# Kernel optimization log

Hardware: AMD Instinct MI355X
Metric: run time of the kernel (lower is better)

## Reference

```python
import jax, jax.numpy as jnp
import numpy as np

SEQ, B, IN_DIM = 100, 2048, 64
MID_I, LATENT, V_MID, V_LAT, MID_O, OUT_DIM = 60, 20, 800, 50, 800, 512


def _lstm_cell(x, h, c, wih, whh, bih, bhh):
    # PyTorch gate order: i, f, g, o
    g = x @ wih.T + h @ whh.T + bih + bhh
    i, f, gg, o = jnp.split(g, 4, axis=-1)
    c = jax.nn.sigmoid(f) * c + jax.nn.sigmoid(i) * jnp.tanh(gg)
    h = jax.nn.sigmoid(o) * jnp.tanh(c)
    return h, c


def _lstm_seq(xs, wih, whh, bih, bhh, hid):
    b = xs.shape[1]
    init = (jnp.zeros((b, hid), xs.dtype), jnp.zeros((b, hid), xs.dtype))
    def step(carry, xt):
        h, c = _lstm_cell(xt, carry[0], carry[1], wih, whh, bih, bhh)
        return (h, c), h
    _, outs = jax.lax.scan(step, init, xs)
    return outs  # (seq, B, hid)


def setup_inputs() -> dict:
    key = jax.random.key(0)
    ks = iter(jax.random.split(key, 40))
    w = lambda shape: jax.random.normal(next(ks), shape, jnp.float32) * 0.05
    p = {}
    p['x'] = jax.random.normal(next(ks), (SEQ, B, IN_DIM), jnp.float32)
    p['fc1_wih'] = w((4 * MID_I, IN_DIM)); p['fc1_whh'] = w((4 * MID_I, MID_I))
    p['fc1_bih'] = w((4 * MID_I,)); p['fc1_bhh'] = w((4 * MID_I,))
    p['fc21_wih'] = w((4 * LATENT, MID_I)); p['fc21_whh'] = w((4 * LATENT, LATENT))
    p['fc21_bih'] = w((4 * LATENT,)); p['fc21_bhh'] = w((4 * LATENT,))
    p['lin1_w'] = w((V_MID, LATENT * SEQ)); p['lin1_b'] = w((V_MID,))
    p['lin2_w'] = w((V_LAT, V_MID)); p['lin2_b'] = w((V_LAT,))
    p['idlin_w'] = w((V_LAT, V_LAT)); p['idlin_b'] = w((V_LAT,))
    p['down1_w'] = w((LATENT, V_LAT)); p['down1_b'] = w((LATENT,))
    p['down2_w'] = w((LATENT, OUT_DIM)); p['down2_b'] = w((LATENT,))
    p['l3_wih'] = w((4 * V_LAT, LATENT)); p['l3_whh'] = w((4 * V_LAT, V_LAT))
    p['l3_bih'] = w((4 * V_LAT,)); p['l3_bhh'] = w((4 * V_LAT,))
    p['l4_wih'] = w((4 * MID_O, V_LAT)); p['l4_whh'] = w((4 * MID_O, MID_O))
    p['l4_bih'] = w((4 * MID_O,)); p['l4_bhh'] = w((4 * MID_O,))
    p['l5_wih'] = w((4 * OUT_DIM, MID_O)); p['l5_whh'] = w((4 * OUT_DIM, OUT_DIM))
    p['l5_bih'] = w((4 * OUT_DIM,)); p['l5_bhh'] = w((4 * OUT_DIM,))
    return p


def reference(x, fc1_wih, fc1_whh, fc1_bih, fc1_bhh,
              fc21_wih, fc21_whh, fc21_bih, fc21_bhh,
              lin1_w, lin1_b, lin2_w, lin2_b,
              idlin_w, idlin_b, down1_w, down1_b, down2_w, down2_b,
              l3_wih, l3_whh, l3_bih, l3_bhh,
              l4_wih, l4_whh, l4_bih, l4_bhh,
              l5_wih, l5_whh, l5_bih, l5_bhh):
    seq, b, _ = x.shape
    # encode
    h1 = jax.nn.relu(_lstm_seq(x, fc1_wih, fc1_whh, fc1_bih, fc1_bhh, MID_I))
    out21 = _lstm_seq(h1, fc21_wih, fc21_whh, fc21_bih, fc21_bhh, LATENT)
    flat = jnp.transpose(out21, (1, 2, 0)).reshape(b, -1)  # (B, latent*seq)
    mu = jax.nn.relu(flat @ lin1_w.T + lin1_b)
    mu = jax.nn.relu(mu @ lin2_w.T + lin2_b)  # (B, v_latent)
    # decode
    h_t = mu
    c_t = mu @ idlin_w.T + idlin_b
    out = mu @ down1_w.T + down1_b
    h2 = jnp.zeros((b, MID_O), mu.dtype); c2 = jnp.zeros((b, MID_O), mu.dtype)
    h3 = jnp.zeros((b, OUT_DIM), mu.dtype); c3 = jnp.zeros((b, OUT_DIM), mu.dtype)
    def step(carry, _):
        h_t, c_t, h2, c2, h3, c3, out = carry
        h_t, c_t = _lstm_cell(out, h_t, c_t, l3_wih, l3_whh, l3_bih, l3_bhh)
        h2, c2 = _lstm_cell(h_t, h2, c2, l4_wih, l4_whh, l4_bih, l4_bhh)
        h3, c3 = _lstm_cell(h2, h3, c3, l5_wih, l5_whh, l5_bih, l5_bhh)
        out = h3 @ down2_w.T + down2_b
        return (h_t, c_t, h2, c2, h3, c3, out), h3
    _, muTheta = jax.lax.scan(step, (h_t, c_t, h2, c2, h3, c3, out), None, length=seq)
    return muTheta, mu
```

## Files before the change

### kernel.cpp

```cpp
#include <hip/hip_runtime.h>
#include <cstdint>
#include <cstddef>

#define SEQ     100
#define BATCH   2048
#define IN_DIM  64
#define MID_I   60
#define LATENT  20
#define V_MID   800
#define V_LAT   50
#define MID_O   800
#define OUT_DIM 512

#define KP4  896
#define KP5  1344
#define KPL1 2048

using f32x4  = __attribute__((ext_vector_type(4))) float;
using u16x8  = __attribute__((ext_vector_type(8))) unsigned short;
using bf16x8 = __attribute__((ext_vector_type(8))) __bf16;
typedef _Float16 f16;
typedef _Float16 f16x8 __attribute__((ext_vector_type(8)));

__device__ __forceinline__ unsigned short f2bf(float x){
    unsigned u = __builtin_bit_cast(unsigned, x);
    u += 0x7FFFu + ((u >> 16) & 1u);
    return (unsigned short)(u >> 16);
}
__device__ __forceinline__ float bf2f(unsigned short b){
    unsigned u = ((unsigned)b) << 16; return __builtin_bit_cast(float, u);
}
__device__ __forceinline__ float sigm(float x){ return 1.f/(1.f+__expf(-x)); }
__device__ __forceinline__ float tanh_f(float x){ return 1.f - 2.f/(__expf(2.f*x)+1.f); }

typedef const __attribute__((address_space(1))) unsigned int* gas_ptr;
typedef __attribute__((address_space(3))) unsigned int* las_ptr;
__device__ __forceinline__ void gld16(const void* g, char* l) {
    __builtin_amdgcn_global_load_lds((gas_ptr)g, (las_ptr)l, 16, 0, 0);
}

constexpr int BM = 64, BN = 64, BK = 16;
template<bool RELU_A1, bool RELU_OUT>
__global__ __launch_bounds__(256)
void gemm2k(const float* __restrict__ A1, int K1,
            const float* __restrict__ A2, int K2,
            const float* __restrict__ W1, const float* __restrict__ W2,
            const float* __restrict__ b1, const float* __restrict__ b2,
            float* __restrict__ C, int M, int N)
{
    __shared__ float As[BK][BM + 1];
    __shared__ float Bs[BK][BN + 1];
    const int tx = threadIdx.x & 15;
    const int ty = threadIdx.x >> 4;
    const int n0 = blockIdx.x * BN;
    const int m0 = blockIdx.y * BM;

    float acc[4][4] = {};

    for (int src = 0; src < 2; ++src) {
        const float* A = src ? A2 : A1;
        const float* W = src ? W2 : W1;
        const int    K = src ? K2 : K1;
        if (A == nullptr || K == 0) continue;
        for (int k0 = 0; k0 < K; k0 += BK) {
            #pragma unroll
            for (int i = 0; i < 4; ++i) {
                int idx = threadIdx.x + i * 256;
                int k = idx & 15, m = idx >> 4;
                int gm = m0 + m, gk = k0 + k;
                float v = 0.f;
                if (gm < M && gk < K) v = A[(size_t)gm * K + gk];
                if (RELU_A1 && src == 0) v = fmaxf(v, 0.f);
                As[k][m] = v;
            }
            #pragma unroll
            for (int i = 0; i < 4; ++i) {
                int idx = threadIdx.x + i * 256;
                int k = idx & 15, n = idx >> 4;
                int gn = n0 + n, gk = k0 + k;
                float v = 0.f;
                if (gn < N && gk < K) v = W[(size_t)gn * K + gk];
                Bs[k][n] = v;
            }
            __syncthreads();
            #pragma unroll
            for (int kk = 0; kk < BK; ++kk) {
                float a[4], b[4];
                #pragma unroll
                for (int i = 0; i < 4; ++i) a[i] = As[kk][ty + i * 16];
                #pragma unroll
                for (int j = 0; j < 4; ++j) b[j] = Bs[kk][tx + j * 16];
                #pragma unroll
                for (int i = 0; i < 4; ++i)
                    #pragma unroll
                    for (int j = 0; j < 4; ++j)
                        acc[i][j] += a[i] * b[j];
            }
            __syncthreads();
        }
    }

    #pragma unroll
    for (int i = 0; i < 4; ++i) {
        int gm = m0 + ty + i * 16;
        if (gm >= M) continue;
        #pragma unroll
        for (int j = 0; j < 4; ++j) {
            int gn = n0 + tx + j * 16;
            if (gn >= N) continue;
            float v = acc[i][j];
            if (b1) v += b1[gn];
            if (b2) v += b2[gn];
            if (RELU_OUT) v = fmaxf(v, 0.f);
            C[(size_t)gm * N + gn] = v;
        }
    }
}

template<bool RELU>
__global__ __launch_bounds__(256, 2)
void gemm_mfma0(const unsigned short* __restrict__ Ah, const unsigned short* __restrict__ Al,
                const unsigned short* __restrict__ Bh, const unsigned short* __restrict__ Bl,
                int Kp, int Nstore, const float* __restrict__ bi, float* __restrict__ Cout)
{
    __shared__ __align__(16) char smem[32768];
    const int tid  = threadIdx.x;
    const int lane = tid & 63;
    const int wid  = tid >> 6;
    const int m0   = blockIdx.y * 128;
    const int n0   = blockIdx.x * 128;
    const int wr   = (wid >> 1) << 6;
    const int wc   = (wid & 1) << 6;
    const int fr   = lane & 15;
    const int fg   = lane >> 4;
    const int slotR = ((fg ^ (fr & 3)) << 4);

    const int r0 = 32 * wid + (lane >> 2);
    const int sl = (((lane & 3) ^ ((lane >> 2) & 3)) << 3);
    const unsigned short* gA0h = Ah + (size_t)(m0 + r0)      * Kp + sl;
    const unsigned short* gA1h = Ah + (size_t)(m0 + r0 + 16) * Kp + sl;
    const unsigned short* gA0l = Al + (size_t)(m0 + r0)      * Kp + sl;
    const unsigned short* gA1l = Al + (size_t)(m0 + r0 + 16) * Kp + sl;
    const unsigned short* gB0h = Bh + (size_t)(n0 + r0)      * Kp + sl;
    const unsigned short* gB1h = Bh + (size_t)(n0 + r0 + 16) * Kp + sl;
    const unsigned short* gB0l = Bl + (size_t)(n0 + r0)      * Kp + sl;
    const unsigned short* gB1l = Bl + (size_t)(n0 + r0 + 16) * Kp + sl;
    char* lA0h = smem +     0 + (2 * wid    ) * 1024;
    char* lA1h = smem +     0 + (2 * wid + 1) * 1024;
    char* lA0l = smem +  8192 + (2 * wid    ) * 1024;
    char* lA1l = smem +  8192 + (2 * wid + 1) * 1024;
    char* lB0h = smem + 16384 + (2 * wid    ) * 1024;
    char* lB1h = smem + 16384 + (2 * wid + 1) * 1024;
    char* lB0l = smem + 24576 + (2 * wid    ) * 1024;
    char* lB1l = smem + 24576 + (2 * wid + 1) * 1024;

    f32x4 acc[4][4];
    #pragma unroll
    for (int i = 0; i < 4; ++i)
        #pragma unroll
        for (int j = 0; j < 4; ++j) acc[i][j] = (f32x4){0.f, 0.f, 0.f, 0.f};

    for (int k0 = 0; k0 < Kp; k0 += 32) {
        __syncthreads();
        gld16(gA0h + k0, lA0h); gld16(gA1h + k0, lA1h);
        gld16(gA0l + k0, lA0l); gld16(gA1l + k0, lA1l);
        gld16(gB0h + k0, lB0h); gld16(gB1h + k0, lB1h);
        gld16(gB0l + k0, lB0l); gld16(gB1l + k0, lB1l);
        __syncthreads();

        bf16x8 ah[4], al[4];
        #pragma unroll
        for (int i = 0; i < 4; ++i) {
            int ro = (wr + i * 16 + fr) * 64 + slotR;
            ah[i] = *(const bf16x8*)(smem +        ro);
            al[i] = *(const bf16x8*)(smem + 8192 + ro);
        }
        #pragma unroll
        for (int j = 0; j < 4; ++j) {
            int ro = (wc + j * 16 + fr) * 64 + slotR;
            bf16x8 fbh = *(const bf16x8*)(smem + 16384 + ro);
            bf16x8 fbl = *(const bf16x8*)(smem + 24576 + ro);
            #pragma unroll
            for (int i = 0; i < 4; ++i) {
                acc[i][j] = __builtin_amdgcn_mfma_f32_16x16x32_bf16(ah[i], fbh, acc[i][j], 0, 0, 0);
                acc[i][j] = __builtin_amdgcn_mfma_f32_16x16x32_bf16(ah[i], fbl, acc[i][j], 0, 0, 0);
                acc[i][j] = __builtin_amdgcn_mfma_f32_16x16x32_bf16(al[i], fbh, acc[i][j], 0, 0, 0);
            }
        }
    }

    #pragma unroll
    for (int j = 0; j < 4; ++j) {
        int gc = n0 + wc + j * 16 + fr;
        if (gc >= Nstore) continue;
        float badd = bi[gc];
        #pragma unroll
        for (int i = 0; i < 4; ++i)
            #pragma unroll
            for (int r = 0; r < 4; ++r) {
                int gr = m0 + wr + i * 16 + fg * 4 + r;
                float v = acc[i][j][r] + badd;
                if (RELU) v = fmaxf(v, 0.f);
                Cout[(size_t)gr * Nstore + gc] = v;
            }
    }
}

template<int MODE>
__global__ __launch_bounds__(256, 3)
void gemm_dec(const f16* __restrict__ A, const f16* __restrict__ W,
              int Kp, int NK, int H, int NBYX,
              const float* __restrict__ bp,
              float* __restrict__ cstate,
              f16* __restrict__ wr1, int st1, int off1,
              f16* __restrict__ wr2, int st2, int off2,
              float* __restrict__ out_t)
{
    __shared__ __align__(16) char smem[49152];
    const int xcd = blockIdx.x & 7;
    const int ii  = blockIdx.x >> 3;
    const int by  = xcd * NBYX + (ii % NBYX);
    const int bx  = ii / NBYX;
    const int m0 = by * 128;
    const int n0 = bx * 128;

    const int tid  = threadIdx.x;
    const int lane = tid & 63;
    const int wid  = tid >> 6;
    const int wm   = wid >> 1;
    const int wn   = wid & 1;
    const int fr   = lane & 15;
    const int fg   = lane >> 4;
    const int swz  = (fg ^ (fr & 3) ^ ((fr >> 2) & 1)) * 16;

    const int rbase = 32 * wid;
    const int lrow  = lane >> 2;
    const int chnk  = (lane & 3) ^ ((lane >> 2) & 3) ^ ((lane >> 4) & 1);
    const f16* sA0 = A + (size_t)(m0 + rbase + lrow)      * Kp + chnk * 8;
    const f16* sA1 = A + (size_t)(m0 + rbase + 16 + lrow) * Kp + chnk * 8;
    const f16* sW0 = W + (size_t)(n0 + rbase + lrow)      * Kp + chnk * 8;
    const f16* sW1 = W + (size_t)(n0 + rbase + 16 + lrow) * Kp + chnk * 8;

    f32x4 acc[4][4];
    #pragma unroll
    for (int i = 0; i < 4; ++i)
        #pragma unroll
        for (int j = 0; j < 4; ++j) acc[i][j] = (f32x4){0.f, 0.f, 0.f, 0.f};

    auto stage = [&](int t, int buf) {
        const int kb = t * 32;
        char* bb = smem + buf * 16384;
        gld16(sA0 + kb, bb + rbase * 64);
        gld16(sA1 + kb, bb + (rbase + 16) * 64);
        gld16(sW0 + kb, bb + 8192 + rbase * 64);
        gld16(sW1 + kb, bb + 8192 + (rbase + 16) * 64);
    };

    stage(0, 0);
    stage(1, 1);

    int buf = 0;
    for (int t = 0; t < NK; ++t) {
        if (t + 1 < NK) asm volatile("s_waitcnt vmcnt(4)" ::: "memory");
        else            asm volatile("s_waitcnt vmcnt(0)" ::: "memory");
        __builtin_amdgcn_s_barrier();
        if (t + 2 < NK) stage(t + 2, (buf + 2) % 3);
        const char* bb = smem + buf * 16384;
        f16x8 af[4];
        #pragma unroll
        for (int i = 0; i < 4; ++i)
            af[i] = *(const f16x8*)(bb + (64 * wm + 16 * i + fr) * 64 + swz);
        #pragma unroll
        for (int j = 0; j < 4; ++j) {
            f16x8 vw = *(const f16x8*)(bb + 8192 + (64 * wn + 16 * j + fr) * 64 + swz);
            #pragma unroll
            for (int i = 0; i < 4; ++i)
                acc[i][j] = __builtin_amdgcn_mfma_f32_16x16x32_f16(af[i], vw, acc[i][j], 0, 0, 0);
        }
        buf = (buf + 1) % 3;
    }

    float* gt = (float*)smem;
    const int u32 = tid & 31;
    const int r8  = tid >> 5;
    const int unit = (n0 >> 2) + u32;
    const f32x4 bv = ((const f32x4*)bp)[unit];

    #pragma unroll
    for (int half = 0; half < 2; ++half) {
        __syncthreads();
        if (wm == half) {
            #pragma unroll
            for (int i = 0; i < 4; ++i)
                #pragma unroll
                for (int j = 0; j < 4; ++j)
                    #pragma unroll
                    for (int r = 0; r < 4; ++r)
                        gt[(16*i + 4*fg + r) * 132 + 64*wn + 16*j + fr] = acc[i][j][r];
        }
        __syncthreads();
        #pragma unroll
        for (int kk = 0; kk < 8; ++kk) {
            const int lr  = 8 * kk + r8;
            const int row = m0 + 64 * half + lr;
            f32x4 g = *(const f32x4*)(gt + lr * 132 + u32 * 4);
            float gi = g[0] + bv[0], gf = g[1] + bv[1];
            float gg = g[2] + bv[2], go = g[3] + bv[3];
            size_t ci = (size_t)row * H + unit;
            float cn = sigm(gf) * cstate[ci] + sigm(gi) * tanh_f(gg);
            float hn = sigm(go) * tanh_f(cn);
            cstate[ci] = cn;
            f16 hh = (f16)hn;
            wr1[(size_t)row * st1 + off1 + unit] = hh;
            if (MODE == 1) wr2[(size_t)row * st2 + off2 + unit] = hh;
            if (MODE == 2) out_t[(size_t)row * H + unit] = hn;
        }
    }
}

__global__ void split_pack_lin1(const float* __restrict__ src,
                                unsigned short* __restrict__ dh, unsigned short* __restrict__ dl)
{
    int idx = blockIdx.x * blockDim.x + threadIdx.x;
    if (idx >= V_MID * LATENT * SEQ) return;
    int n = idx / (LATENT * SEQ), c = idx - n * (LATENT * SEQ);
    int l = c / SEQ, s = c - l * SEQ;
    float x = src[idx];
    unsigned short h = f2bf(x);
    size_t d = (size_t)n * KPL1 + s * LATENT + l;
    dh[d] = h;
    dl[d] = f2bf(x - bf2f(h));
}

__global__ void split_pack_rows(const float* __restrict__ src, int total, int K, int Kp,
                                unsigned short* __restrict__ dh, unsigned short* __restrict__ dl)
{
    int idx = blockIdx.x * blockDim.x + threadIdx.x;
    if (idx >= total) return;
    int n = idx / K, k = idx - n * K;
    float x = src[idx];
    unsigned short h = f2bf(x);
    size_t d = (size_t)n * Kp + k;
    dh[d] = h;
    dl[d] = f2bf(x - bf2f(h));
}

__global__ void pack_f16(const float* __restrict__ src, int total, int K, int Kp,
                         int coff, int HU, f16* __restrict__ dh)
{
    int idx = blockIdx.x * blockDim.x + threadIdx.x;
    if (idx >= total) return;
    int n = idx / K, k = idx - n * K;
    int p = (n % HU) * 4 + n / HU;
    dh[(size_t)p * Kp + coff + k] = (f16)src[idx];
}

__global__ void pack_flat_f16(const float* __restrict__ src, int total, f16* __restrict__ d)
{
    int idx = blockIdx.x * blockDim.x + threadIdx.x;
    if (idx < total) d[idx] = (f16)src[idx];
}

__global__ void bias_pack(const float* __restrict__ bih, const float* __restrict__ bhh,
                          int H, float* __restrict__ bp)
{
    int idx = blockIdx.x * blockDim.x + threadIdx.x;
    if (idx >= 4 * H) return;
    int g = idx / H, u = idx - g * H;
    bp[u * 4 + g] = bih[idx] + bhh[idx];
}

__global__ void bias_sum(const float* __restrict__ a, const float* __restrict__ b,
                         int n, float* __restrict__ d)
{
    int idx = blockIdx.x * blockDim.x + threadIdx.x;
    if (idx < n) d[idx] = a[idx] + b[idx];
}

__global__ __launch_bounds__(256)
void enc_rec1(const float* __restrict__ xp, int T,
              const float* __restrict__ whh,
              float* __restrict__ hbuf, float* __restrict__ cbuf,
              unsigned short* __restrict__ h1h, unsigned short* __restrict__ h1l)
{
    __shared__ float Wt[60][240];
    __shared__ float hs[4][60];
    for (int idx = threadIdx.x; idx < 240 * 60; idx += 256) {
        int n = idx / 60, k = idx % 60;
        Wt[k][n] = whh[idx];
    }
    int wid = threadIdx.x >> 6, lane = threadIdx.x & 63;
    int b = blockIdx.x * 4 + wid;
    float h = 0.f, c = 0.f;
    if (lane < 60) {
        h = hbuf[(size_t)b * 60 + lane];
        c = cbuf[(size_t)b * 60 + lane];
        hs[wid][lane] = h;
    }
    __syncthreads();
    for (int t = 0; t < T; ++t) {
        if (lane < 60) {
            const float* xr = xp + ((size_t)t * BATCH + b) * 240;
            float gi = xr[lane], gf = xr[60 + lane], gg = xr[120 + lane], go = xr[180 + lane];
            for (int k = 0; k < 60; ++k) {
                float v = hs[wid][k];
                gi += v * Wt[k][lane];
                gf += v * Wt[k][60 + lane];
                gg += v * Wt[k][120 + lane];
                go += v * Wt[k][180 + lane];
            }
            float cn = sigm(gf) * c + sigm(gi) * tanh_f(gg);
            float hn = sigm(go) * tanh_f(cn);
            c = cn; h = hn;
            float rh = fmaxf(hn, 0.f);
            unsigned short hh = f2bf(rh);
            size_t d = ((size_t)t * BATCH + b) * 64 + lane;
            h1h[d] = hh;
            h1l[d] = f2bf(rh - bf2f(hh));
        }
        __syncthreads();
        if (lane < 60) hs[wid][lane] = h;
        __syncthreads();
    }
    if (lane < 60) {
        hbuf[(size_t)b * 60 + lane] = h;
        cbuf[(size_t)b * 60 + lane] = c;
    }
}

__global__ __launch_bounds__(256)
void enc_rec21(const float* __restrict__ xp, int T, int t0,
               const float* __restrict__ whh,
               float* __restrict__ hbuf, float* __restrict__ cbuf,
               unsigned short* __restrict__ fh, unsigned short* __restrict__ fl)
{
    __shared__ float Wt[20][80];
    __shared__ float hs[4][20];
    for (int idx = threadIdx.x; idx < 80 * 20; idx += 256) {
        int n = idx / 20, k = idx % 20;
        Wt[k][n] = whh[idx];
    }
    int wid = threadIdx.x >> 6, lane = threadIdx.x & 63;
    int b = blockIdx.x * 4 + wid;
    float h = 0.f, c = 0.f;
    if (lane < 20) {
        h = hbuf[(size_t)b * 20 + lane];
        c = cbuf[(size_t)b * 20 + lane];
        hs[wid][lane] = h;
    }
    __syncthreads();
    for (int t = 0; t < T; ++t) {
        if (lane < 20) {
            const float* xr = xp + ((size_t)t * BATCH + b) * 80;
            float gi = xr[lane], gf = xr[20 + lane], gg = xr[40 + lane], go = xr[60 + lane];
            for (int k = 0; k < 20; ++k) {
                float v = hs[wid][k];
                gi += v * Wt[k][lane];
                gf += v * Wt[k][20 + lane];
                gg += v * Wt[k][40 + lane];
                go += v * Wt[k][60 + lane];
            }
            float cn = sigm(gf) * c + sigm(gi) * tanh_f(gg);
            float hn = sigm(go) * tanh_f(cn);
            c = cn; h = hn;
            int col = (t0 + t) * 20 + lane;
            unsigned short hh = f2bf(hn);
            fh[(size_t)b * KPL1 + col] = hh;
            fl[(size_t)b * KPL1 + col] = f2bf(hn - bf2f(hh));
        }
        __syncthreads();
        if (lane < 20) hs[wid][lane] = h;
        __syncthreads();
    }
    if (lane < 20) {
        hbuf[(size_t)b * 20 + lane] = h;
        cbuf[(size_t)b * 20 + lane] = c;
    }
}

__global__ __launch_bounds__(256)
void dec_l3(const float* __restrict__ outb,
            const float* __restrict__ wih,
            const float* __restrict__ whh,
            const float* __restrict__ bih, const float* __restrict__ bhh,
            float* __restrict__ h_t, float* __restrict__ c_t,
            f16* __restrict__ a4)
{
    __shared__ float Wt[70][200];
    __shared__ float xin[4][70];
    for (int idx = threadIdx.x; idx < 200 * 20; idx += 256) {
        int n = idx / 20, k = idx % 20;
        Wt[k][n] = wih[idx];
    }
    for (int idx = threadIdx.x; idx < 200 * 50; idx += 256) {
        int n = idx / 50, k = idx % 50;
        Wt[20 + k][n] = whh[idx];
    }
    int wid = threadIdx.x >> 6, lane = threadIdx.x & 63;
    int b = blockIdx.x * 4 + wid;
    if (lane < 20) xin[wid][lane]      = outb[(size_t)b * 20 + lane];
    if (lane < 50) xin[wid][20 + lane] = h_t[(size_t)b * 50 + lane];
    __syncthreads();
    if (lane < 50) {
        float gi = bih[lane] + bhh[lane];
        float gf = bih[50 + lane] + bhh[50 + lane];
        float gg = bih[100 + lane] + bhh[100 + lane];
        float go = bih[150 + lane] + bhh[150 + lane];
        for (int k = 0; k < 70; ++k) {
            float v = xin[wid][k];
            gi += v * Wt[k][lane];
            gf += v * Wt[k][50 + lane];
            gg += v * Wt[k][100 + lane];
            go += v * Wt[k][150 + lane];
        }
        float cold = c_t[(size_t)b * 50 + lane];
        float cn = sigm(gf) * cold + sigm(gi) * tanh_f(gg);
        float hn = sigm(go) * tanh_f(cn);
        c_t[(size_t)b * 50 + lane] = cn;
        h_t[(size_t)b * 50 + lane] = hn;
        a4[(size_t)b * KP4 + lane] = (f16)hn;
    }
}

__global__ __launch_bounds__(512)
void dec_step3(const float* __restrict__ h3prev,
               const f16* __restrict__ w2p, const float* __restrict__ b2,
               const float* __restrict__ wih, const float* __restrict__ whh,
               const float* __restrict__ bih, const float* __restrict__ bhh,
               float* __restrict__ h_t, float* __restrict__ c_t,
               f16* __restrict__ a4)
{
    __shared__ f16   w2s[20][512];
    __shared__ float W3[70][200];
    __shared__ float xb[8][80];
    const int tid  = threadIdx.x;
    const int lane = tid & 63;
    const int w    = tid >> 6;
    const int row  = blockIdx.x * 8 + w;

    for (int idx = tid; idx < 20 * 512; idx += 512)
        w2s[idx >> 9][idx & 511] = w2p[idx];
    for (int idx = tid; idx < 200 * 20; idx += 512) {
        int n = idx / 20, k = idx - n * 20;
        W3[k][n] = wih[idx];
    }
    for (int idx = tid; idx < 200 * 50; idx += 512) {
        int n = idx / 50, k = idx - n * 50;
        W3[20 + k][n] = whh[idx];
    }
    if (lane < 50) xb[w][20 + lane] = h_t[(size_t)row * 50 + lane];

    float hreg[8];
    const float* hrow = h3prev + (size_t)row * 512;
    #pragma unroll
    for (int c = 0; c < 8; ++c) hreg[c] = hrow[lane + 64 * c];
    __syncthreads();

    #pragma unroll 4
    for (int n = 0; n < 20; ++n) {
        float s = 0.f;
        #pragma unroll
        for (int c = 0; c < 8; ++c) s += hreg[c] * (float)w2s[n][lane + 64 * c];
        #pragma unroll
        for (int o = 32; o; o >>= 1) s += __shfl_xor(s, o);
        if (lane == 0) xb[w][n] = s + b2[n];
    }
    __syncthreads();

    if (lane < 50) {
        const int u = lane;
        float gi = bih[u] + bhh[u];
        float gf = bih[50 + u] + bhh[50 + u];
        float gg = bih[100 + u] + bhh[100 + u];
        float go = bih[150 + u] + bhh[150 + u];
        for (int k = 0; k < 70; ++k) {
            float v = xb[w][k];
            gi += v * W3[k][u];
            gf += v * W3[k][50 + u];
            gg += v * W3[k][100 + u];
            go += v * W3[k][150 + u];
        }
        size_t ci = (size_t)row * 50 + u;
        float cn = sigm(gf) * c_t[ci] + sigm(gi) * tanh_f(gg);
        float hn = sigm(go) * tanh_f(cn);
        c_t[ci] = cn;
        h_t[ci] = hn;
        a4[(size_t)row * KP4 + u] = (f16)hn;
    }
}

extern "C" void kernel_launch(void* const* d_in, const int* in_sizes, int n_in,
                              void* d_out_v, int out_size, void* d_ws, size_t ws_size,
                              hipStream_t stream)
{
    const float* x        = (const float*)d_in[0];
    const float* fc1_wih  = (const float*)d_in[1];
    const float* fc1_whh  = (const float*)d_in[2];
    const float* fc1_bih  = (const float*)d_in[3];
    const float* fc1_bhh  = (const float*)d_in[4];
    const float* fc21_wih = (const float*)d_in[5];
    const float* fc21_whh = (const float*)d_in[6];
    const float* fc21_bih = (const float*)d_in[7];
    const float* fc21_bhh = (const float*)d_in[8];
    const float* lin1_w   = (const float*)d_in[9];
    const float* lin1_b   = (const float*)d_in[10];
    const float* lin2_w   = (const float*)d_in[11];
    const float* lin2_b   = (const float*)d_in[12];
    const float* idlin_w  = (const float*)d_in[13];
    const float* idlin_b  = (const float*)d_in[14];
    const float* down1_w  = (const float*)d_in[15];
    const float* down1_b  = (const float*)d_in[16];
    const float* down2_w  = (const float*)d_in[17];
    const float* down2_b  = (const float*)d_in[18];
    const float* l3_wih   = (const float*)d_in[19];
    const float* l3_whh   = (const float*)d_in[20];
    const float* l3_bih   = (const float*)d_in[21];
    const float* l3_bhh   = (const float*)d_in[22];
    const float* l4_wih   = (const float*)d_in[23];
    const float* l4_whh   = (const float*)d_in[24];
    const float* l4_bih   = (const float*)d_in[25];
    const float* l4_bhh   = (const float*)d_in[26];
    const float* l5_wih   = (const float*)d_in[27];
    const float* l5_whh   = (const float*)d_in[28];
    const float* l5_bih   = (const float*)d_in[29];
    const float* l5_bhh   = (const float*)d_in[30];
    float* out = (float*)d_out_v;

    char* base = (char*)d_ws;
    size_t off = 0;
    auto alloc = [&](size_t bytes) -> void* {
        off = (off + 255) & ~(size_t)255;
        void* p = base + off;
        off += bytes;
        return p;
    };

    size_t us_begin = (off + 255) & ~(size_t)255;
    f16* W4h = (f16*)alloc((size_t)3200 * KP4 * 2);
    f16* W5h = (f16*)alloc((size_t)2048 * KP5 * 2);
    unsigned short* L1h = (unsigned short*)alloc((size_t)896 * KPL1 * 2);
    unsigned short* L1l = (unsigned short*)alloc((size_t)896 * KPL1 * 2);
    unsigned short* Fh  = (unsigned short*)alloc((size_t)BATCH * KPL1 * 2);
    unsigned short* Fl  = (unsigned short*)alloc((size_t)BATCH * KPL1 * 2);
    unsigned short* Fc1h  = (unsigned short*)alloc((size_t)256 * 64 * 2);
    unsigned short* Fc1l  = (unsigned short*)alloc((size_t)256 * 64 * 2);
    unsigned short* Fc21h = (unsigned short*)alloc((size_t)128 * 64 * 2);
    unsigned short* Fc21l = (unsigned short*)alloc((size_t)128 * 64 * 2);
    const int CH = 20;
    unsigned short* H1h = (unsigned short*)alloc((size_t)CH * BATCH * 64 * 2);
    unsigned short* H1l = (unsigned short*)alloc((size_t)CH * BATCH * 64 * 2);
    f16* A4[2]; f16* A5[2];
    for (int p = 0; p < 2; ++p) {
        A4[p] = (f16*)alloc((size_t)BATCH * KP4 * 2);
        A5[p] = (f16*)alloc((size_t)BATCH * KP5 * 2);
    }
    size_t us_end = off;

    size_t fz_begin = (off + 255) & ~(size_t)255;
    float* c2   = (float*)alloc((size_t)BATCH * MID_O * 4);
    float* c3   = (float*)alloc((size_t)BATCH * OUT_DIM * 4);
    float* hb1  = (float*)alloc((size_t)BATCH * MID_I * 4);
    float* cb1  = (float*)alloc((size_t)BATCH * MID_I * 4);
    float* hb21 = (float*)alloc((size_t)BATCH * LATENT * 4);
    float* cb21 = (float*)alloc((size_t)BATCH * LATENT * 4);
    size_t fz_end = off;

    float* bp4   = (float*)alloc((size_t)4 * MID_O * 4);
    float* bp5   = (float*)alloc((size_t)4 * OUT_DIM * 4);
    float* bs1   = (float*)alloc((size_t)4 * MID_I * 4);
    float* bs21  = (float*)alloc((size_t)4 * LATENT * 4);
    f16*   w2p   = (f16*)alloc((size_t)LATENT * OUT_DIM * 2);
    float* mu1   = (float*)alloc((size_t)BATCH * V_MID * 4);
    float* mu    = (float*)alloc((size_t)BATCH * V_LAT * 4);
    float* h_t   = (float*)alloc((size_t)BATCH * V_LAT * 4);
    float* c_t   = (float*)alloc((size_t)BATCH * V_LAT * 4);
    float* outb  = (float*)alloc((size_t)BATCH * LATENT * 4);
    unsigned short* Xh = (unsigned short*)alloc((size_t)SEQ * BATCH * 64 * 2);
    unsigned short* Xl = (unsigned short*)alloc((size_t)SEQ * BATCH * 64 * 2);
    float* xp1c  = (float*)alloc((size_t)CH * BATCH * 4 * MID_I * 4);
    float* xp21c = (float*)alloc((size_t)CH * BATCH * 4 * LATENT * 4);

    hipMemsetAsync(base + us_begin, 0, us_end - us_begin, stream);
    hipMemsetAsync(base + fz_begin, 0, fz_end - fz_begin, stream);

    pack_f16<<<(3200 * 50  + 255) / 256, 256, 0, stream>>>(l4_wih, 3200 * 50,  50,  KP4, 0,   800, W4h);
    pack_f16<<<(3200 * 800 + 255) / 256, 256, 0, stream>>>(l4_whh, 3200 * 800, 800, KP4, 64,  800, W4h);
    pack_f16<<<(2048 * 800 + 255) / 256, 256, 0, stream>>>(l5_wih, 2048 * 800, 800, KP5, 0,   512, W5h);
    pack_f16<<<(2048 * 512 + 255) / 256, 256, 0, stream>>>(l5_whh, 2048 * 512, 512, KP5, 832, 512, W5h);
    split_pack_lin1<<<(V_MID * LATENT * SEQ + 255) / 256, 256, 0, stream>>>(lin1_w, L1h, L1l);
    split_pack_rows<<<(240 * 64 + 255) / 256, 256, 0, stream>>>(fc1_wih, 240 * 64, 64, 64, Fc1h, Fc1l);
    split_pack_rows<<<(80 * 60 + 255) / 256, 256, 0, stream>>>(fc21_wih, 80 * 60, 60, 64, Fc21h, Fc21l);
    split_pack_rows<<<(SEQ * BATCH * 64 + 255) / 256, 256, 0, stream>>>(x, SEQ * BATCH * 64, 64, 64, Xh, Xl);
    pack_flat_f16<<<(LATENT * OUT_DIM + 255) / 256, 256, 0, stream>>>(down2_w, LATENT * OUT_DIM, w2p);
    bias_pack<<<(4 * MID_O   + 255) / 256, 256, 0, stream>>>(l4_bih, l4_bhh, MID_O,   bp4);
    bias_pack<<<(4 * OUT_DIM + 255) / 256, 256, 0, stream>>>(l5_bih, l5_bhh, OUT_DIM, bp5);
    bias_sum<<<1, 256, 0, stream>>>(fc1_bih, fc1_bhh, 4 * MID_I, bs1);
    bias_sum<<<1, 256, 0, stream>>>(fc21_bih, fc21_bhh, 4 * LATENT, bs21);

    for (int c0 = 0; c0 < SEQ; c0 += CH) {
        {
            dim3 g(2, CH * BATCH / 128);
            gemm_mfma0<false><<<g, 256, 0, stream>>>(
                Xh + (size_t)c0 * BATCH * 64, Xl + (size_t)c0 * BATCH * 64,
                Fc1h, Fc1l, 64, 4 * MID_I, bs1, xp1c);
        }
        enc_rec1<<<BATCH / 4, 256, 0, stream>>>(xp1c, CH, fc1_whh, hb1, cb1, H1h, H1l);
        {
            dim3 g(1, CH * BATCH / 128);
            gemm_mfma0<false><<<g, 256, 0, stream>>>(
                H1h, H1l, Fc21h, Fc21l, 64, 4 * LATENT, bs21, xp21c);
        }
        enc_rec21<<<BATCH / 4, 256, 0, stream>>>(xp21c, CH, c0, fc21_whh, hb21, cb21, Fh, Fl);
    }

    {
        dim3 g(7, 16);
        gemm_mfma0<true><<<g, 256, 0, stream>>>(Fh, Fl, L1h, L1l, KPL1, V_MID, lin1_b, mu1);
    }
    {
        dim3 g((V_LAT + BN - 1) / BN, BATCH / BM);
        gemm2k<false, true><<<g, 256, 0, stream>>>(mu1, V_MID, nullptr, 0,
            lin2_w, nullptr, lin2_b, nullptr, mu, BATCH, V_LAT);
    }

    hipMemcpyAsync(h_t, mu, (size_t)BATCH * V_LAT * 4, hipMemcpyDeviceToDevice, stream);
    {
        dim3 g(1, BATCH / BM);
        gemm2k<false, false><<<g, 256, 0, stream>>>(mu, V_LAT, nullptr, 0,
            idlin_w, nullptr, idlin_b, nullptr, c_t, BATCH, V_LAT);
        gemm2k<false, false><<<g, 256, 0, stream>>>(mu, V_LAT, nullptr, 0,
            down1_w, nullptr, down1_b, nullptr, outb, BATCH, LATENT);
    }

    for (int t = 0; t < SEQ; ++t) {
        const int p = t & 1;
        if (t == 0) {
            dec_l3<<<BATCH / 4, 256, 0, stream>>>(outb, l3_wih, l3_whh, l3_bih, l3_bhh,
                                                  h_t, c_t, A4[0]);
        } else {
            dec_step3<<<BATCH / 8, 512, 0, stream>>>(
                out + (size_t)(t - 1) * BATCH * OUT_DIM,
                w2p, down2_b, l3_wih, l3_whh, l3_bih, l3_bhh,
                h_t, c_t, A4[p]);
        }
        {
            gemm_dec<1><<<dim3(400), 256, 0, stream>>>(
                A4[p], W4h, KP4, KP4 / 32, MID_O, 2, bp4, c2,
                A4[p ^ 1], KP4, 64,
                A5[p], KP5, 0,
                nullptr);
        }
        {
            gemm_dec<2><<<dim3(256), 256, 0, stream>>>(
                A5[p], W5h, KP5, KP5 / 32, OUT_DIM, 2, bp5, c3,
                A5[p ^ 1], KP5, 832,
                nullptr, 0, 0,
                out + (size_t)t * BATCH * OUT_DIM);
        }
    }

    hipMemcpyAsync(out + (size_t)SEQ * BATCH * OUT_DIM, mu,
                   (size_t)BATCH * V_LAT * 4, hipMemcpyDeviceToDevice, stream);
}
```

Baseline: 7.518 ms.

## Fuse down2 projection into last-arriving l5 GEMM block per row tile

The down2 projection (h3 @ down2_w.T) moves out of the per-step l3 kernel and into the tail of the l5 gemm_dec kernel. Blocks count their arrivals with an atomic counter per row tile, and the last block of each tile computes the 20-wide output for its 128 rows. The l3 cell becomes a lighter kernel that reads a prepacked f16 transposed weight and handles 16 rows per block. This removes the redundant per-block reload of the h3 row and of the down2 weights in the old step kernel. It adds threadfence/atomic ordering and a serial tail done by one block per tile, and l3 weights are now rounded to f16.

```diff
diff --git a/kernel.cpp b/kernel.cpp
--- a/kernel.cpp
+++ b/kernel.cpp
@@ -214,7 +214,9 @@
               float* __restrict__ cstate,
               f16* __restrict__ wr1, int st1, int off1,
               f16* __restrict__ wr2, int st2, int off2,
-              float* __restrict__ out_t)
+              float* __restrict__ out_t,
+              const f16* __restrict__ w2p, const float* __restrict__ b2d,
+              float* __restrict__ outb, int* __restrict__ cnt)
 {
     __shared__ __align__(16) char smem[49152];
     const int xcd = blockIdx.x & 7;
@@ -316,6 +318,82 @@
             if (MODE == 2) out_t[(size_t)row * H + unit] = hn;
         }
     }
+
+    if (MODE == 2) {
+        __threadfence();
+        __syncthreads();
+        int* wflag = (int*)(smem + 40960);
+        if (tid == 0) {
+            int old = atomicAdd(cnt + by, 1);
+            *wflag = (((old + 1) & 15) == 0);
+        }
+        __syncthreads();
+        if (!*wflag) return;
+        __threadfence();
+
+        f16* w2s = (f16*)smem;
+        for (int idx = tid; idx < 20 * 512; idx += 256) w2s[idx] = w2p[idx];
+        __syncthreads();
+        for (int e = tid; e < 128 * 20; e += 256) {
+            int r = e / 20, n = e - (e / 20) * 20;
+            const float* hrow = out_t + (size_t)(m0 + r) * OUT_DIM;
+            const f16* wn2 = w2s + n * 512;
+            float s = b2d[n];
+            #pragma unroll 4
+            for (int k = 0; k < 512; k += 8) {
+                f32x4 h0 = *(const f32x4*)(hrow + k);
+                f32x4 h1 = *(const f32x4*)(hrow + k + 4);
+                s += h0[0]*(float)wn2[k]   + h0[1]*(float)wn2[k+1]
+                   + h0[2]*(float)wn2[k+2] + h0[3]*(float)wn2[k+3]
+                   + h1[0]*(float)wn2[k+4] + h1[1]*(float)wn2[k+5]
+                   + h1[2]*(float)wn2[k+6] + h1[3]*(float)wn2[k+7];
+            }
+            outb[(size_t)(m0 + r) * LATENT + n] = s;
+        }
+    }
+}
+
+__global__ __launch_bounds__(512)
+void l3k(const float* __restrict__ outb, const f16* __restrict__ W3p,
+         const float* __restrict__ bih, const float* __restrict__ bhh,
+         float* __restrict__ h_t, float* __restrict__ c_t,
+         f16* __restrict__ a4next)
+{
+    __shared__ f16 W3s[70 * 200];
+    __shared__ float xb[16][72];
+    const int tid = threadIdx.x;
+    const int r0 = blockIdx.x * 16;
+    for (int idx = tid; idx < 70 * 200; idx += 512) W3s[idx] = W3p[idx];
+    for (int idx = tid; idx < 16 * 20; idx += 512) {
+        int r = idx / 20, n = idx - (idx / 20) * 20;
+        xb[r][n] = outb[(size_t)(r0 + r) * LATENT + n];
+    }
+    for (int idx = tid; idx < 16 * 50; idx += 512) {
+        int r = idx / 50, u = idx - (idx / 50) * 50;
+        xb[r][20 + u] = h_t[(size_t)(r0 + r) * 50 + u];
+    }
+    __syncthreads();
+    for (int e = tid; e < 16 * 50; e += 512) {
+        int r = e / 50, u = e - (e / 50) * 50;
+        float gi = bih[u] + bhh[u];
+        float gf = bih[50 + u] + bhh[50 + u];
+        float gg = bih[100 + u] + bhh[100 + u];
+        float go = bih[150 + u] + bhh[150 + u];
+        for (int k = 0; k < 70; ++k) {
+            float v = xb[r][k];
+            const f16* wk = W3s + k * 200;
+            gi += v * (float)wk[u];
+            gf += v * (float)wk[50 + u];
+            gg += v * (float)wk[100 + u];
+            go += v * (float)wk[150 + u];
+        }
+        size_t ci = (size_t)(r0 + r) * 50 + u;
+        float cn = sigm(gf) * c_t[ci] + sigm(gi) * tanh_f(gg);
+        float hn = sigm(go) * tanh_f(cn);
+        c_t[ci] = cn;
+        h_t[ci] = hn;
+        a4next[(size_t)(r0 + r) * KP4 + u] = (f16)hn;
+    }
 }
 
 __global__ void split_pack_lin1(const float* __restrict__ src,
@@ -359,6 +437,16 @@
 {
     int idx = blockIdx.x * blockDim.x + threadIdx.x;
     if (idx < total) d[idx] = (f16)src[idx];
+}
+
+__global__ void pack_l3(const float* __restrict__ wih, const float* __restrict__ whh,
+                        f16* __restrict__ W3p)
+{
+    int idx = blockIdx.x * blockDim.x + threadIdx.x;
+    if (idx >= 70 * 200) return;
+    int k = idx / 200, n = idx - k * 200;
+    float v = (k < 20) ? wih[n * 20 + k] : whh[n * 50 + (k - 20)];
+    W3p[idx] = (f16)v;
 }
 
 __global__ void bias_pack(const float* __restrict__ bih, const float* __restrict__ bhh,
@@ -519,73 +607,6 @@
         c_t[(size_t)b * 50 + lane] = cn;
         h_t[(size_t)b * 50 + lane] = hn;
         a4[(size_t)b * KP4 + lane] = (f16)hn;
-    }
-}
-
-__global__ __launch_bounds__(512)
-void dec_step3(const float* __restrict__ h3prev,
-               const f16* __restrict__ w2p, const float* __restrict__ b2,
-               const float* __restrict__ wih, const float* __restrict__ whh,
-               const float* __restrict__ bih, const float* __restrict__ bhh,
-               float* __restrict__ h_t, float* __restrict__ c_t,
-               f16* __restrict__ a4)
-{
-    __shared__ f16   w2s[20][512];
-    __shared__ float W3[70][200];
-    __shared__ float xb[8][80];
-    const int tid  = threadIdx.x;
-    const int lane = tid & 63;
-    const int w    = tid >> 6;
-    const int row  = blockIdx.x * 8 + w;
-
-    for (int idx = tid; idx < 20 * 512; idx += 512)
-        w2s[idx >> 9][idx & 511] = w2p[idx];
-    for (int idx = tid; idx < 200 * 20; idx += 512) {
-        int n = idx / 20, k = idx - n * 20;
-        W3[k][n] = wih[idx];
-    }
-    for (int idx = tid; idx < 200 * 50; idx += 512) {
-        int n = idx / 50, k = idx - n * 50;
-        W3[20 + k][n] = whh[idx];
-    }
-    if (lane < 50) xb[w][20 + lane] = h_t[(size_t)row * 50 + lane];
-
-    float hreg[8];
-    const float* hrow = h3prev + (size_t)row * 512;
-    #pragma unroll
-    for (int c = 0; c < 8; ++c) hreg[c] = hrow[lane + 64 * c];
-    __syncthreads();
-
-    #pragma unroll 4
-    for (int n = 0; n < 20; ++n) {
-        float s = 0.f;
-        #pragma unroll
-        for (int c = 0; c < 8; ++c) s += hreg[c] * (float)w2s[n][lane + 64 * c];
-        #pragma unroll
-        for (int o = 32; o; o >>= 1) s += __shfl_xor(s, o);
-        if (lane == 0) xb[w][n] = s + b2[n];
-    }
-    __syncthreads();
-
-    if (lane < 50) {
-        const int u = lane;
-        float gi = bih[u] + bhh[u];
-        float gf = bih[50 + u] + bhh[50 + u];
-        float gg = bih[100 + u] + bhh[100 + u];
-        float go = bih[150 + u] + bhh[150 + u];
-        for (int k = 0; k < 70; ++k) {
-            float v = xb[w][k];
-            gi += v * W3[k][u];
-            gf += v * W3[k][50 + u];
-            gg += v * W3[k][100 + u];
-            go += v * W3[k][150 + u];
-        }
-        size_t ci = (size_t)row * 50 + u;
-        float cn = sigm(gf) * c_t[ci] + sigm(gi) * tanh_f(gg);
-        float hn = sigm(go) * tanh_f(cn);
-        c_t[ci] = cn;
-        h_t[ci] = hn;
-        a4[(size_t)row * KP4 + u] = (f16)hn;
     }
 }
 
@@ -665,11 +686,13 @@
     float* cb21 = (float*)alloc((size_t)BATCH * LATENT * 4);
     size_t fz_end = off;
 
+    int*   cnt   = (int*)alloc(16 * 4);
     float* bp4   = (float*)alloc((size_t)4 * MID_O * 4);
     float* bp5   = (float*)alloc((size_t)4 * OUT_DIM * 4);
     float* bs1   = (float*)alloc((size_t)4 * MID_I * 4);
     float* bs21  = (float*)alloc((size_t)4 * LATENT * 4);
     f16*   w2p   = (f16*)alloc((size_t)LATENT * OUT_DIM * 2);
+    f16*   W3p   = (f16*)alloc((size_t)70 * 200 * 2);
     float* mu1   = (float*)alloc((size_t)BATCH * V_MID * 4);
     float* mu    = (float*)alloc((size_t)BATCH * V_LAT * 4);
     float* h_t   = (float*)alloc((size_t)BATCH * V_LAT * 4);
@@ -692,6 +715,7 @@
     split_pack_rows<<<(80 * 60 + 255) / 256, 256, 0, stream>>>(fc21_wih, 80 * 60, 60, 64, Fc21h, Fc21l);
     split_pack_rows<<<(SEQ * BATCH * 64 + 255) / 256, 256, 0, stream>>>(x, SEQ * BATCH * 64, 64, 64, Xh, Xl);
     pack_flat_f16<<<(LATENT * OUT_DIM + 255) / 256, 256, 0, stream>>>(down2_w, LATENT * OUT_DIM, w2p);
+    pack_l3<<<(70 * 200 + 255) / 256, 256, 0, stream>>>(l3_wih, l3_whh, W3p);
     bias_pack<<<(4 * MID_O   + 255) / 256, 256, 0, stream>>>(l4_bih, l4_bhh, MID_O,   bp4);
     bias_pack<<<(4 * OUT_DIM + 255) / 256, 256, 0, stream>>>(l5_bih, l5_bhh, OUT_DIM, bp5);
     bias_sum<<<1, 256, 0, stream>>>(fc1_bih, fc1_bhh, 4 * MID_I, bs1);
@@ -738,24 +762,24 @@
             dec_l3<<<BATCH / 4, 256, 0, stream>>>(outb, l3_wih, l3_whh, l3_bih, l3_bhh,
                                                   h_t, c_t, A4[0]);
         } else {
-            dec_step3<<<BATCH / 8, 512, 0, stream>>>(
-                out + (size_t)(t - 1) * BATCH * OUT_DIM,
-                w2p, down2_b, l3_wih, l3_whh, l3_bih, l3_bhh,
-                h_t, c_t, A4[p]);
+            l3k<<<BATCH / 16, 512, 0, stream>>>(outb, W3p, l3_bih, l3_bhh,
+                                                h_t, c_t, A4[p]);
         }
         {
             gemm_dec<1><<<dim3(400), 256, 0, stream>>>(
                 A4[p], W4h, KP4, KP4 / 32, MID_O, 2, bp4, c2,
                 A4[p ^ 1], KP4, 64,
                 A5[p], KP5, 0,
-                nullptr);
+                nullptr,
+                nullptr, nullptr, nullptr, nullptr);
         }
         {
             gemm_dec<2><<<dim3(256), 256, 0, stream>>>(
                 A5[p], W5h, KP5, KP5 / 32, OUT_DIM, 2, bp5, c3,
                 A5[p ^ 1], KP5, 832,
                 nullptr, 0, 0,
-                out + (size_t)t * BATCH * OUT_DIM);
+                out + (size_t)t * BATCH * OUT_DIM,
+                w2p, down2_b, outb, cnt);
         }
     }
 
```

Measured after the change: 16.26 ms. 2.16x slower.
